# Performance work log

Measured on AMD Instinct MI355X. Metric: run time of the kernel, lower is better.

## Reference

```python
import jax, jax.numpy as jnp
import numpy as np

L, B, T, S, W, H = 4, 2, 2048, 512, 512, 8  # layers, batch, n_ctx, cond units, width, heads
CH = W // H


def _ln(x, g, b):
    m = x.mean(-1, keepdims=True)
    v = ((x - m) ** 2).mean(-1, keepdims=True)
    return (x - m) * jax.lax.rsqrt(v + 1e-5) * g + b


def setup_inputs() -> dict:
    key = jax.random.key(0)
    ks = jax.random.split(key, 16)
    std = 0.25 * np.sqrt(1.0 / W)  # init_scale * sqrt(1/width), as in Transformer.__init__
    f32 = jnp.float32
    d = {
        "x": jax.random.normal(ks[0], (B, T, W), f32),
        "cond_k": jax.random.normal(ks[1], (B, S, W), f32),
        "cond_v": jax.random.normal(ks[2], (B, S, W), f32),
        # stacked per-layer params; weights stored [in, out] (torch Linear transposed)
        "qkv_w": jax.random.normal(ks[3], (L, W, 3 * W), f32) * std,
        "qkv_b": jnp.zeros((L, 3 * W), f32),
        "attn_proj_w": jax.random.normal(ks[4], (L, W, W), f32) * std,
        "attn_proj_b": jnp.zeros((L, W), f32),
        "cross_proj_w": jax.random.normal(ks[5], (L, W, W), f32) * std,
        "cross_proj_b": jnp.zeros((L, W), f32),
        "fc_w": jax.random.normal(ks[6], (L, W, 4 * W), f32) * std,
        "fc_b": jnp.zeros((L, 4 * W), f32),
        "mlp_proj_w": jax.random.normal(ks[7], (L, 4 * W, W), f32) * std,
        "mlp_proj_b": jnp.zeros((L, W), f32),
        "ln1_g": jnp.ones((L, W), f32), "ln1_b": jnp.zeros((L, W), f32),
        "ln3_g": jnp.ones((L, W), f32), "ln3_b": jnp.zeros((L, W), f32),
        "ln4_g": jnp.ones((L, W), f32), "ln4_b": jnp.zeros((L, W), f32),
    }
    return d


def reference(x, cond_k, cond_v, qkv_w, qkv_b, attn_proj_w, attn_proj_b,
              cross_proj_w, cross_proj_b, fc_w, fc_b, mlp_proj_w, mlp_proj_b,
              ln1_g, ln1_b, ln3_g, ln3_b, ln4_g, ln4_b):
    b, t, w = x.shape
    ch = w // H
    scale = 1.0 / np.sqrt(np.sqrt(ch))  # applied to both q and k, as in torch code
    kk = cond_k.reshape(b, -1, H, ch)
    vv = cond_v.reshape(b, -1, H, ch)
    n_layers = qkv_w.shape[0]
    for i in range(n_layers):
        # ---- self-attention ----
        h = _ln(x, ln1_g[i], ln1_b[i])
        qkv = (h @ qkv_w[i] + qkv_b[i]).reshape(b, t, H, 3 * ch)
        q, k, v = qkv[..., :ch], qkv[..., ch:2 * ch], qkv[..., 2 * ch:]
        wts = jnp.einsum('bthc,bshc->bhts', q * scale, k * scale)
        wts = jax.nn.softmax(wts.astype(jnp.float32), axis=-1).astype(wts.dtype)
        a = jnp.einsum('bhts,bshc->bthc', wts, v).reshape(b, t, w)
        x = x + a @ attn_proj_w[i] + attn_proj_b[i]
        # ---- cross-attention (q is ln_3(x) directly, no q projection) ----
        h = _ln(x, ln3_g[i], ln3_b[i])
        q = h.reshape(b, t, H, ch)
        wts = jnp.einsum('bthc,bshc->bhts', q * scale, kk * scale)
        wts = jax.nn.softmax(wts.astype(jnp.float32), axis=-1).astype(wts.dtype)
        a = jnp.einsum('bhts,bshc->bthc', wts, vv).reshape(b, t, w)
        x = x + a @ cross_proj_w[i] + cross_proj_b[i]
        # ---- MLP (exact erf GELU, as torch nn.GELU default) ----
        h = _ln(x, ln4_g[i], ln4_b[i])
        h = jax.nn.gelu(h @ fc_w[i] + fc_b[i], approximate=False)
        x = x + h @ mlp_proj_w[i] + mlp_proj_b[i]
    return x
```

## Files before the change

kernel.cpp:

```cpp
#include <hip/hip_runtime.h>
#include <hip/hip_bf16.h>
#include <cstdint>


typedef __bf16 bf16;
typedef __bf16 bf16x8 __attribute__((ext_vector_type(8)));
typedef float f32x4 __attribute__((ext_vector_type(4)));

#define AS1(p) ((__attribute__((address_space(1))) void*)(uintptr_t)(p))
#define AS3(p) ((__attribute__((address_space(3))) void*)(p))

__device__ __forceinline__ unsigned short bf2us(bf16 v) {
    return __builtin_bit_cast(unsigned short, v);
}

template <int N>
__device__ __forceinline__ void vmbar() {
    if constexpr (N == 0)      asm volatile("s_waitcnt vmcnt(0)\n\ts_barrier" ::: "memory");
    else if constexpr (N == 2) asm volatile("s_waitcnt vmcnt(2)\n\ts_barrier" ::: "memory");
    else if constexpr (N == 5) asm volatile("s_waitcnt vmcnt(5)\n\ts_barrier" ::: "memory");
    else if constexpr (N == 6) asm volatile("s_waitcnt vmcnt(6)\n\ts_barrier" ::: "memory");
    else if constexpr (N == 8) asm volatile("s_waitcnt vmcnt(8)\n\ts_barrier" ::: "memory");
    __builtin_amdgcn_sched_barrier(0);
}
__device__ __forceinline__ void plainbar() {
    asm volatile("s_barrier" ::: "memory");
    __builtin_amdgcn_sched_barrier(0);
}

__global__ __launch_bounds__(256) void ln_kernel(const float* __restrict__ x,
                                                 const float* __restrict__ gam,
                                                 const float* __restrict__ bet,
                                                 bf16* __restrict__ h) {
    int row  = blockIdx.x * 4 + (threadIdx.x >> 6);
    int lane = threadIdx.x & 63;
    const float4* xr = (const float4*)(x + (size_t)row * 512) + lane * 2;
    float4 a = xr[0], b = xr[1];
    float s  = a.x + a.y + a.z + a.w + b.x + b.y + b.z + b.w;
    float ss = a.x * a.x + a.y * a.y + a.z * a.z + a.w * a.w +
               b.x * b.x + b.y * b.y + b.z * b.z + b.w * b.w;
#pragma unroll
    for (int off = 1; off < 64; off <<= 1) {
        s  += __shfl_xor(s, off);
        ss += __shfl_xor(ss, off);
    }
    float mean = s * (1.f / 512.f);
    float var  = ss * (1.f / 512.f) - mean * mean;
    float rstd = rsqrtf(fmaxf(var, 0.f) + 1e-5f);
    const float4* gr = (const float4*)gam + lane * 2;
    const float4* br = (const float4*)bet + lane * 2;
    float4 g0 = gr[0], g1 = gr[1], b0 = br[0], b1 = br[1];
    bf16x8 hv;
    hv[0] = (bf16)((a.x - mean) * rstd * g0.x + b0.x);
    hv[1] = (bf16)((a.y - mean) * rstd * g0.y + b0.y);
    hv[2] = (bf16)((a.z - mean) * rstd * g0.z + b0.z);
    hv[3] = (bf16)((a.w - mean) * rstd * g0.w + b0.w);
    hv[4] = (bf16)((b.x - mean) * rstd * g1.x + b1.x);
    hv[5] = (bf16)((b.y - mean) * rstd * g1.y + b1.y);
    hv[6] = (bf16)((b.z - mean) * rstd * g1.z + b1.z);
    hv[7] = (bf16)((b.w - mean) * rstd * g1.w + b1.w);
    *(bf16x8*)(h + (size_t)row * 512 + lane * 8) = hv;
}

__global__ void wtrans_kernel(const float* __restrict__ in, bf16* __restrict__ out,
                              int K, int N) {
    __shared__ float tile[32][33];
    int n0 = blockIdx.x * 32, k0 = blockIdx.y * 32;
    const float* ip = in + (size_t)blockIdx.z * K * N;
    bf16* op = out + (size_t)blockIdx.z * N * K;
#pragma unroll
    for (int i = threadIdx.y; i < 32; i += 8)
        tile[i][threadIdx.x] = ip[(size_t)(k0 + i) * N + n0 + threadIdx.x];
    __syncthreads();
#pragma unroll
    for (int i = threadIdx.y; i < 32; i += 8)
        op[(size_t)(n0 + i) * K + k0 + threadIdx.x] = (bf16)tile[threadIdx.x][i];
}

__global__ void cvt_kernel(const float* __restrict__ in, bf16* __restrict__ out, int n) {
    int i = (blockIdx.x * 256 + threadIdx.x) * 8;
    if (i + 8 <= n) {
        const float4* p = (const float4*)(in + i);
        float4 a = p[0], b = p[1];
        bf16x8 v;
        v[0] = (bf16)a.x; v[1] = (bf16)a.y; v[2] = (bf16)a.z; v[3] = (bf16)a.w;
        v[4] = (bf16)b.x; v[5] = (bf16)b.y; v[6] = (bf16)b.z; v[7] = (bf16)b.w;
        *(bf16x8*)(out + i) = v;
    }
}

__global__ __launch_bounds__(256) void vtrans_self(const bf16* __restrict__ qkvb,
                                                   bf16* __restrict__ VTs, int T_) {
    __shared__ bf16 tl[64][66];
    int tb = blockIdx.x * 64;
    int bh = blockIdx.y;
    int b = bh >> 3, h = bh & 7;
    int tid = threadIdx.x;
#pragma unroll
    for (int e = 0; e < 2; ++e) {
        int idx = e * 256 + tid;
        int t = idx >> 3, ci = (idx & 7) * 8;
        bf16x8 v = *(const bf16x8*)(qkvb + ((size_t)b * T_ + tb + t) * 1536 +
                                    h * 192 + 128 + ci);
#pragma unroll
        for (int j = 0; j < 8; ++j) tl[ci + j][t] = v[j];
    }
    __syncthreads();
#pragma unroll
    for (int e = 0; e < 2; ++e) {
        int idx = e * 256 + tid;
        int ch = idx >> 3, ti = (idx & 7) * 8;
        bf16x8 v;
#pragma unroll
        for (int j = 0; j < 8; ++j) v[j] = tl[ch][ti + j];
        *(bf16x8*)(VTs + ((size_t)bh * 64 + ch) * T_ + tb + ti) = v;
    }
}

__global__ __launch_bounds__(256) void vtrans_cross(const float* __restrict__ cv,
                                                    bf16* __restrict__ VTc, int S_) {
    __shared__ bf16 tl[64][66];
    int sb = blockIdx.x * 64;
    int bh = blockIdx.y;
    int b = bh >> 3, h = bh & 7;
    int tid = threadIdx.x;
#pragma unroll
    for (int e = 0; e < 4; ++e) {
        int idx = e * 256 + tid;
        int s = idx >> 4, ci = (idx & 15) * 4;
        float4 v = *(const float4*)(cv + ((size_t)b * S_ + sb + s) * 512 + h * 64 + ci);
        tl[ci + 0][s] = (bf16)v.x; tl[ci + 1][s] = (bf16)v.y;
        tl[ci + 2][s] = (bf16)v.z; tl[ci + 3][s] = (bf16)v.w;
    }
    __syncthreads();
#pragma unroll
    for (int e = 0; e < 2; ++e) {
        int idx = e * 256 + tid;
        int ch = idx >> 3, si = (idx & 7) * 8;
        bf16x8 v;
#pragma unroll
        for (int j = 0; j < 8; ++j) v[j] = tl[ch][si + j];
        *(bf16x8*)(VTc + ((size_t)bh * 64 + ch) * S_ + sb + si) = v;
    }
}

template <int EPI, int BM>
__global__ __launch_bounds__(256) void gemm_kernel(const bf16* __restrict__ A,
                                                   const bf16* __restrict__ Bt,
                                                   const float* __restrict__ bias,
                                                   const float* res, void* out,
                                                   int M, int N, int K) {
    constexpr int MI = BM / 32;
    constexpr int LPW = BM / 32 + 4;
    constexpr int ABYTES = BM * 128;
    __shared__ __align__(16) bf16 As[2 * BM * 64];
    __shared__ __align__(16) bf16 Bs[2 * 128 * 64];
    int tiles_n = N >> 7;
    int bid = blockIdx.x;
    int cpx = gridDim.x >> 3;
    bid = (bid & 7) * cpx + (bid >> 3);
    int bm = bid / tiles_n, bn = bid % tiles_n;
    int tid = threadIdx.x, wave = tid >> 6, lane = tid & 63;
    int wm = wave >> 1, wn = wave & 1;
    int g = lane >> 4, cc = lane & 15;
    f32x4 acc[MI][4] = {};
    const bf16* Ag = A + (size_t)(bm * BM) * K;
    const bf16* Bg = Bt + (size_t)(bn << 7) * K;
    int scol = (tid & 7) * 8;

    auto stage = [&](int k0, int buf) {
#pragma unroll
        for (int e = 0; e < BM / 32; ++e) {
            int row = (e * 256 + tid) >> 3;
            __builtin_amdgcn_global_load_lds(AS1(Ag + (size_t)row * K + k0 + scol),
                                             AS3((char*)As + buf * ABYTES + e * 4096 + wave * 1024),
                                             16, 0, 0);
        }
#pragma unroll
        for (int e = 0; e < 4; ++e) {
            int row = (e * 256 + tid) >> 3;
            __builtin_amdgcn_global_load_lds(AS1(Bg + (size_t)row * K + k0 + scol),
                                             AS3((char*)Bs + buf * 16384 + e * 4096 + wave * 1024),
                                             16, 0, 0);
        }
    };

    int nk = K >> 6;
    stage(0, 0);
    stage(64, 1);
    for (int t = 0; t < nk; ++t) {
        if (t + 1 < nk) vmbar<LPW>(); else vmbar<0>();
        const bf16* Ab = As + (t & 1) * (BM * 64);
        const bf16* Bb = Bs + (t & 1) * (128 * 64);
#pragma unroll
        for (int kk = 0; kk < 2; ++kk) {
            bf16x8 af[MI], bfr[4];
#pragma unroll
            for (int mi = 0; mi < MI; ++mi)
                af[mi] = *(const bf16x8*)(Ab + (wm * (BM / 2) + mi * 16 + cc) * 64 + kk * 32 + g * 8);
#pragma unroll
            for (int ni = 0; ni < 4; ++ni)
                bfr[ni] = *(const bf16x8*)(Bb + (wn * 64 + ni * 16 + cc) * 64 + kk * 32 + g * 8);
#pragma unroll
            for (int mi = 0; mi < MI; ++mi)
#pragma unroll
                for (int ni = 0; ni < 4; ++ni)
                    acc[mi][ni] = __builtin_amdgcn_mfma_f32_16x16x32_bf16(
                        af[mi], bfr[ni], acc[mi][ni], 0, 0, 0);
        }
        plainbar();
        if (t + 2 < nk) stage((t + 2) * 64, t & 1);
    }
    int m0 = bm * BM + wm * (BM / 2);
    int n0 = (bn << 7) + wn * 64;
#pragma unroll
    for (int ni = 0; ni < 4; ++ni) {
        int n = n0 + ni * 16 + cc;
        float bv = bias[n];
#pragma unroll
        for (int mi = 0; mi < MI; ++mi) {
#pragma unroll
            for (int r = 0; r < 4; ++r) {
                int m = m0 + mi * 16 + g * 4 + r;
                float v = acc[mi][ni][r] + bv;
                if (EPI == 1) v = 0.5f * v * (1.f + erff(v * 0.70710678118654752f));
                if (EPI == 2)
                    ((float*)out)[(size_t)m * N + n] = res[(size_t)m * N + n] + v;
                else
                    ((bf16*)out)[(size_t)m * N + n] = (bf16)v;
            }
        }
    }
}

__global__ __launch_bounds__(512) void attn_kernel(
    const bf16* __restrict__ Qp, int q_rs, int q_hs,
    const bf16* __restrict__ Kp, int k_rs, int k_hs,
    const bf16* __restrict__ Vt, int vt_s,
    bf16* __restrict__ Op, int T_, int S_) {
    __shared__ __align__(16) char SM[40960];

    int numQ = T_ >> 6;
    int phys = blockIdx.x;
    int cpx = gridDim.x >> 3;
    int bid = (phys & 7) * cpx + (phys >> 3);
    int qb = bid % numQ;
    int bh = bid / numQ;
    int b = bh >> 3, h = bh & 7;
    int tid = threadIdx.x, wave = tid >> 6, lane = tid & 63;
    int wq = wave >> 1, ws = wave & 1;
    int g = lane >> 4, cc = lane & 15;
    int qrow0 = qb * 64;
    int swz = (cc >> 1) & 3;

    const bf16* Qb = Qp + ((size_t)b * T_ + qrow0 + wq * 16) * q_rs + h * q_hs;
    const bf16* Kb = Kp + ((size_t)b * S_) * k_rs + h * k_hs;
    const bf16* Vtb = Vt + (size_t)bh * 64 * vt_s;

    const float QSC = 0.125f * 1.44269504088896f;
    bf16x8 qf[2];
#pragma unroll
    for (int kk = 0; kk < 2; ++kk) {
        bf16x8 raw = *(const bf16x8*)(Qb + (size_t)cc * q_rs + kk * 32 + g * 8);
        bf16x8 sc;
#pragma unroll
        for (int j = 0; j < 8; ++j) sc[j] = (bf16)((float)raw[j] * QSC);
        qf[kk] = sc;
    }

    float l_acc = 0.f;
    f32x4 o_acc[4] = {};
    char* Pw = SM + 32768 + wave * 1024;

    auto stage = [&](int s0, int buf) {
        int row = tid >> 3, cp = tid & 7;
        int col = (cp ^ (row & 7)) * 8;
        __builtin_amdgcn_global_load_lds(AS1(Kb + (size_t)(s0 + row) * k_rs + col),
                                         AS3(SM + buf * 8192 + wave * 1024), 16, 0, 0);
        __builtin_amdgcn_global_load_lds(AS1(Vtb + (size_t)row * vt_s + s0 + col),
                                         AS3(SM + 16384 + buf * 8192 + wave * 1024), 16, 0, 0);
    };

    int nt = S_ >> 6;
    stage(0, 0);
    stage(64, 1);
    for (int t = 0; t < nt; ++t) {
        if (t + 1 < nt) vmbar<2>(); else vmbar<0>();
        char* kbc = SM + (t & 1) * 8192;
        char* vbc = SM + 16384 + (t & 1) * 8192;
        f32x4 sf[2] = {};
        __builtin_amdgcn_s_setprio(1);
#pragma unroll
        for (int kk = 0; kk < 2; ++kk)
#pragma unroll
            for (int sn = 0; sn < 2; ++sn) {
                int row = ws * 32 + sn * 16 + cc;
                bf16x8 kf = *(const bf16x8*)(kbc + row * 128 + (((kk * 4 + g) ^ (cc & 7)) << 4));
                sf[sn] = __builtin_amdgcn_mfma_f32_16x16x32_bf16(kf, qf[kk], sf[sn], 0, 0, 0);
            }
        __builtin_amdgcn_s_setprio(0);
#pragma unroll
        for (int sn = 0; sn < 2; ++sn) {
            float p0 = exp2f(sf[sn][0]), p1 = exp2f(sf[sn][1]);
            float p2 = exp2f(sf[sn][2]), p3 = exp2f(sf[sn][3]);
            l_acc += (p0 + p1) + (p2 + p3);
            uint32_t u01 = (uint32_t)bf2us((bf16)p0) | ((uint32_t)bf2us((bf16)p1) << 16);
            uint32_t u23 = (uint32_t)bf2us((bf16)p2) | ((uint32_t)bf2us((bf16)p3) << 16);
            char* pb = Pw + cc * 64 + (((sn * 2 + (g >> 1)) ^ swz) << 4) + (g & 1) * 8;
            uint2 uu; uu.x = u01; uu.y = u23;
            *(uint2*)pb = uu;
        }
        __builtin_amdgcn_s_setprio(1);
        bf16x8 pa = *(const bf16x8*)(Pw + cc * 64 + ((g ^ swz) << 4));
#pragma unroll
        for (int ni = 0; ni < 4; ++ni) {
            int vrow = ni * 16 + cc;
            bf16x8 vf = *(const bf16x8*)(vbc + vrow * 128 + (((ws * 4 + g) ^ (cc & 7)) << 4));
            o_acc[ni] = __builtin_amdgcn_mfma_f32_16x16x32_bf16(pa, vf, o_acc[ni], 0, 0, 0);
        }
        __builtin_amdgcn_s_setprio(0);
        plainbar();
        if (t + 2 < nt) stage((t + 2) * 64, t & 1);
    }

    l_acc += __shfl_xor(l_acc, 16);
    l_acc += __shfl_xor(l_acc, 32);
    float* sco = (float*)SM;
    float* lf = (float*)(SM + 32768);
    float* scw = sco + wave * 1024;
#pragma unroll
    for (int ni = 0; ni < 4; ++ni)
#pragma unroll
        for (int r = 0; r < 4; ++r)
            scw[(4 * g + r) * 64 + ni * 16 + cc] = o_acc[ni][r];
    if (g == 0) lf[wave * 16 + cc] = l_acc;
    __syncthreads();
    int q = tid >> 3, c0 = (tid & 7) * 8;
    int wqq = q >> 4, qr = q & 15;
    float l = lf[(wqq * 2) * 16 + qr] + lf[(wqq * 2 + 1) * 16 + qr];
    float inv = 1.f / l;
    const float* p0p = sco + (wqq * 2) * 1024 + qr * 64 + c0;
    const float* p1p = sco + (wqq * 2 + 1) * 1024 + qr * 64 + c0;
    bf16x8 o1;
#pragma unroll
    for (int e = 0; e < 2; ++e) {
        float4 v0 = *(const float4*)(p0p + e * 4);
        float4 v1 = *(const float4*)(p1p + e * 4);
        o1[e * 4 + 0] = (bf16)((v0.x + v1.x) * inv);
        o1[e * 4 + 1] = (bf16)((v0.y + v1.y) * inv);
        o1[e * 4 + 2] = (bf16)((v0.z + v1.z) * inv);
        o1[e * 4 + 3] = (bf16)((v0.w + v1.w) * inv);
    }
    *(bf16x8*)(Op + ((size_t)b * T_ + qrow0 + q) * 512 + h * 64 + c0) = o1;
}

extern "C" void kernel_launch(void* const* d_in, const int* in_sizes, int n_in,
                              void* d_out, int out_size, void* d_ws, size_t ws_size,
                              hipStream_t stream) {
    const float* x_in    = (const float*)d_in[0];
    const float* cond_k  = (const float*)d_in[1];
    const float* cond_v  = (const float*)d_in[2];
    const float* qkv_w   = (const float*)d_in[3];
    const float* qkv_b   = (const float*)d_in[4];
    const float* attn_w  = (const float*)d_in[5];
    const float* attn_b  = (const float*)d_in[6];
    const float* cross_w = (const float*)d_in[7];
    const float* cross_b = (const float*)d_in[8];
    const float* fc_w    = (const float*)d_in[9];
    const float* fc_b    = (const float*)d_in[10];
    const float* mlp_w   = (const float*)d_in[11];
    const float* mlp_b   = (const float*)d_in[12];
    const float* ln1_g   = (const float*)d_in[13];
    const float* ln1_b   = (const float*)d_in[14];
    const float* ln3_g   = (const float*)d_in[15];
    const float* ln3_b   = (const float*)d_in[16];
    const float* ln4_g   = (const float*)d_in[17];
    const float* ln4_b   = (const float*)d_in[18];

    const int L = 4, T = 2048, S = 512, W = 512;
    const int M = 2 * T;

    char* ws = (char*)d_ws;
    size_t off = 0;
    auto carve = [&](size_t bytes) -> char* {
        char* p = ws + off;
        off += (bytes + 255) & ~(size_t)255;
        return p;
    };
    bf16* wqkv  = (bf16*)carve((size_t)L * 1536 * 512 * 2);
    bf16* wattn = (bf16*)carve((size_t)L * 512 * 512 * 2);
    bf16* wcrs  = (bf16*)carve((size_t)L * 512 * 512 * 2);
    bf16* wfc   = (bf16*)carve((size_t)L * 2048 * 512 * 2);
    bf16* wmlp  = (bf16*)carve((size_t)L * 512 * 2048 * 2);
    bf16* ckb   = (bf16*)carve((size_t)2 * S * W * 2);
    bf16* VTs   = (bf16*)carve((size_t)16 * 64 * T * 2);
    bf16* VTc   = (bf16*)carve((size_t)16 * 64 * S * 2);
    bf16* hbuf  = (bf16*)carve((size_t)M * 512 * 2);
    bf16* qkvb  = (bf16*)carve((size_t)M * 1536 * 2);
    bf16* abuf  = (bf16*)carve((size_t)M * 512 * 2);
    bf16* fcb   = (bf16*)carve((size_t)M * 2048 * 2);

    dim3 tb(32, 8);
    wtrans_kernel<<<dim3(1536 / 32, 512 / 32, L), tb, 0, stream>>>(qkv_w, wqkv, 512, 1536);
    wtrans_kernel<<<dim3(512 / 32, 512 / 32, L), tb, 0, stream>>>(attn_w, wattn, 512, 512);
    wtrans_kernel<<<dim3(512 / 32, 512 / 32, L), tb, 0, stream>>>(cross_w, wcrs, 512, 512);
    wtrans_kernel<<<dim3(2048 / 32, 512 / 32, L), tb, 0, stream>>>(fc_w, wfc, 512, 2048);
    wtrans_kernel<<<dim3(512 / 32, 2048 / 32, L), tb, 0, stream>>>(mlp_w, wmlp, 2048, 512);
    cvt_kernel<<<(2 * S * W) / 2048, 256, 0, stream>>>(cond_k, ckb, 2 * S * W);
    vtrans_cross<<<dim3(S / 64, 16), 256, 0, stream>>>(cond_v, VTc, S);

    float* x = (float*)d_out;
    hipMemcpyAsync(x, (const void*)x_in, (size_t)M * W * sizeof(float),
                   hipMemcpyDeviceToDevice, stream);

    const int nAttn = 16 * (T / 64);
    for (int i = 0; i < L; ++i) {
        ln_kernel<<<M / 4, 256, 0, stream>>>(x, ln1_g + i * 512, ln1_b + i * 512, hbuf);
        gemm_kernel<0, 64><<<(M / 64) * (1536 / 128), 256, 0, stream>>>(
            hbuf, wqkv + (size_t)i * 1536 * 512, qkv_b + i * 1536, nullptr, qkvb,
            M, 1536, 512);
        vtrans_self<<<dim3(T / 64, 16), 256, 0, stream>>>(qkvb, VTs, T);
        attn_kernel<<<nAttn, 512, 0, stream>>>(
            qkvb, 1536, 192, qkvb + 64, 1536, 192, VTs, T,
            abuf, T, T);
        gemm_kernel<2, 32><<<(M / 32) * (512 / 128), 256, 0, stream>>>(
            abuf, wattn + (size_t)i * 512 * 512, attn_b + i * 512, x, x,
            M, 512, 512);
        ln_kernel<<<M / 4, 256, 0, stream>>>(x, ln3_g + i * 512, ln3_b + i * 512, hbuf);
        attn_kernel<<<nAttn, 512, 0, stream>>>(
            hbuf, 512, 64, ckb, 512, 64, VTc, S,
            abuf, T, S);
        gemm_kernel<2, 32><<<(M / 32) * (512 / 128), 256, 0, stream>>>(
            abuf, wcrs + (size_t)i * 512 * 512, cross_b + i * 512, x, x,
            M, 512, 512);
        ln_kernel<<<M / 4, 256, 0, stream>>>(x, ln4_g + i * 512, ln4_b + i * 512, hbuf);
        gemm_kernel<1, 128><<<(M / 128) * (2048 / 128), 256, 0, stream>>>(
            hbuf, wfc + (size_t)i * 2048 * 512, fc_b + i * 2048, nullptr, fcb,
            M, 2048, 512);
        gemm_kernel<2, 32><<<(M / 32) * (512 / 128), 256, 0, stream>>>(
            fcb, wmlp + (size_t)i * 512 * 2048, mlp_b + i * 512, x, x,
            M, 512, 2048);
    }
}
```

Measured before the change: 639.0 us.

## Restructure cross-attention wave tiling to share K/V fragments across two query tiles

Measured after the change: 645.9 us. About the same (+1.1%).

```diff
diff --git a/kernel.cpp b/kernel.cpp
--- a/kernel.cpp
+++ b/kernel.cpp
@@ -17,7 +17,6 @@
 template <int N>
 __device__ __forceinline__ void vmbar() {
     if constexpr (N == 0)      asm volatile("s_waitcnt vmcnt(0)\n\ts_barrier" ::: "memory");
-    else if constexpr (N == 2) asm volatile("s_waitcnt vmcnt(2)\n\ts_barrier" ::: "memory");
     else if constexpr (N == 5) asm volatile("s_waitcnt vmcnt(5)\n\ts_barrier" ::: "memory");
     else if constexpr (N == 6) asm volatile("s_waitcnt vmcnt(6)\n\ts_barrier" ::: "memory");
     else if constexpr (N == 8) asm volatile("s_waitcnt vmcnt(8)\n\ts_barrier" ::: "memory");
@@ -25,6 +24,10 @@
 }
 __device__ __forceinline__ void plainbar() {
     asm volatile("s_barrier" ::: "memory");
+    __builtin_amdgcn_sched_barrier(0);
+}
+__device__ __forceinline__ void ldsbar() {
+    asm volatile("s_waitcnt lgkmcnt(0)\n\ts_barrier" ::: "memory");
     __builtin_amdgcn_sched_barrier(0);
 }
 
@@ -248,29 +251,31 @@
     int bh = bid / numQ;
     int b = bh >> 3, h = bh & 7;
     int tid = threadIdx.x, wave = tid >> 6, lane = tid & 63;
-    int wq = wave >> 1, ws = wave & 1;
+    int wq = wave >> 2, ws = wave & 3;
+    int sh = ws >> 1, nh = ws & 1;
     int g = lane >> 4, cc = lane & 15;
     int qrow0 = qb * 64;
-    int swz = (cc >> 1) & 3;
-
-    const bf16* Qb = Qp + ((size_t)b * T_ + qrow0 + wq * 16) * q_rs + h * q_hs;
+
+    const bf16* Qb = Qp + ((size_t)b * T_ + qrow0 + wq * 32) * q_rs + h * q_hs;
     const bf16* Kb = Kp + ((size_t)b * S_) * k_rs + h * k_hs;
     const bf16* Vtb = Vt + (size_t)bh * 64 * vt_s;
+    char* PB = SM + 32768;
 
     const float QSC = 0.125f * 1.44269504088896f;
-    bf16x8 qf[2];
-#pragma unroll
-    for (int kk = 0; kk < 2; ++kk) {
-        bf16x8 raw = *(const bf16x8*)(Qb + (size_t)cc * q_rs + kk * 32 + g * 8);
-        bf16x8 sc;
-#pragma unroll
-        for (int j = 0; j < 8; ++j) sc[j] = (bf16)((float)raw[j] * QSC);
-        qf[kk] = sc;
-    }
-
-    float l_acc = 0.f;
-    f32x4 o_acc[4] = {};
-    char* Pw = SM + 32768 + wave * 1024;
+    bf16x8 qf[2][2];
+#pragma unroll
+    for (int qn = 0; qn < 2; ++qn)
+#pragma unroll
+        for (int kk = 0; kk < 2; ++kk) {
+            bf16x8 raw = *(const bf16x8*)(Qb + (size_t)(qn * 16 + cc) * q_rs + kk * 32 + g * 8);
+            bf16x8 sc;
+#pragma unroll
+            for (int j = 0; j < 8; ++j) sc[j] = (bf16)((float)raw[j] * QSC);
+            qf[qn][kk] = sc;
+        }
+
+    float l_acc[2] = {0.f, 0.f};
+    f32x4 o_acc[2][2] = {};
 
     auto stage = [&](int s0, int buf) {
         int row = tid >> 3, cp = tid & 7;
@@ -281,66 +286,89 @@
                                          AS3(SM + 16384 + buf * 8192 + wave * 1024), 16, 0, 0);
     };
 
+    stage(0, 0);
+    __syncthreads();
+
     int nt = S_ >> 6;
-    stage(0, 0);
-    stage(64, 1);
+    int cur = 0;
     for (int t = 0; t < nt; ++t) {
-        if (t + 1 < nt) vmbar<2>(); else vmbar<0>();
-        char* kbc = SM + (t & 1) * 8192;
-        char* vbc = SM + 16384 + (t & 1) * 8192;
+        if (t + 1 < nt) stage((t + 1) * 64, cur ^ 1);
+        char* kbc = SM + cur * 8192;
+        char* vbc = SM + 16384 + cur * 8192;
         f32x4 sf[2] = {};
         __builtin_amdgcn_s_setprio(1);
 #pragma unroll
-        for (int kk = 0; kk < 2; ++kk)
-#pragma unroll
-            for (int sn = 0; sn < 2; ++sn) {
-                int row = ws * 32 + sn * 16 + cc;
-                bf16x8 kf = *(const bf16x8*)(kbc + row * 128 + (((kk * 4 + g) ^ (cc & 7)) << 4));
-                sf[sn] = __builtin_amdgcn_mfma_f32_16x16x32_bf16(kf, qf[kk], sf[sn], 0, 0, 0);
-            }
+        for (int kk = 0; kk < 2; ++kk) {
+            int krow = ws * 16 + cc;
+            bf16x8 kf = *(const bf16x8*)(kbc + krow * 128 + (((kk * 4 + g) ^ (krow & 7)) << 4));
+#pragma unroll
+            for (int qn = 0; qn < 2; ++qn)
+                sf[qn] = __builtin_amdgcn_mfma_f32_16x16x32_bf16(kf, qf[qn][kk], sf[qn], 0, 0, 0);
+        }
         __builtin_amdgcn_s_setprio(0);
 #pragma unroll
-        for (int sn = 0; sn < 2; ++sn) {
-            float p0 = exp2f(sf[sn][0]), p1 = exp2f(sf[sn][1]);
-            float p2 = exp2f(sf[sn][2]), p3 = exp2f(sf[sn][3]);
-            l_acc += (p0 + p1) + (p2 + p3);
+        for (int qn = 0; qn < 2; ++qn) {
+            float p0 = exp2f(sf[qn][0]), p1 = exp2f(sf[qn][1]);
+            float p2 = exp2f(sf[qn][2]), p3 = exp2f(sf[qn][3]);
+            l_acc[qn] += (p0 + p1) + (p2 + p3);
             uint32_t u01 = (uint32_t)bf2us((bf16)p0) | ((uint32_t)bf2us((bf16)p1) << 16);
             uint32_t u23 = (uint32_t)bf2us((bf16)p2) | ((uint32_t)bf2us((bf16)p3) << 16);
-            char* pb = Pw + cc * 64 + (((sn * 2 + (g >> 1)) ^ swz) << 4) + (g & 1) * 8;
+            int prow = wq * 32 + qn * 16 + cc;
+            int chunk = ws * 2 + (g >> 1);
+            char* pb = PB + prow * 128 + ((chunk ^ (prow & 7)) << 4) + (g & 1) * 8;
             uint2 uu; uu.x = u01; uu.y = u23;
             *(uint2*)pb = uu;
         }
+        ldsbar();
         __builtin_amdgcn_s_setprio(1);
-        bf16x8 pa = *(const bf16x8*)(Pw + cc * 64 + ((g ^ swz) << 4));
-#pragma unroll
-        for (int ni = 0; ni < 4; ++ni) {
-            int vrow = ni * 16 + cc;
-            bf16x8 vf = *(const bf16x8*)(vbc + vrow * 128 + (((ws * 4 + g) ^ (cc & 7)) << 4));
-            o_acc[ni] = __builtin_amdgcn_mfma_f32_16x16x32_bf16(pa, vf, o_acc[ni], 0, 0, 0);
-        }
+        bf16x8 pa[2], vf[2];
+#pragma unroll
+        for (int qn = 0; qn < 2; ++qn) {
+            int prow = wq * 32 + qn * 16 + cc;
+            pa[qn] = *(const bf16x8*)(PB + prow * 128 + (((sh * 4 + g) ^ (prow & 7)) << 4));
+        }
+#pragma unroll
+        for (int nj = 0; nj < 2; ++nj) {
+            int vrow = (nh * 2 + nj) * 16 + cc;
+            vf[nj] = *(const bf16x8*)(vbc + vrow * 128 + (((sh * 4 + g) ^ (vrow & 7)) << 4));
+        }
+#pragma unroll
+        for (int qn = 0; qn < 2; ++qn)
+#pragma unroll
+            for (int nj = 0; nj < 2; ++nj)
+                o_acc[qn][nj] = __builtin_amdgcn_mfma_f32_16x16x32_bf16(
+                    pa[qn], vf[nj], o_acc[qn][nj], 0, 0, 0);
         __builtin_amdgcn_s_setprio(0);
-        plainbar();
-        if (t + 2 < nt) stage((t + 2) * 64, t & 1);
-    }
-
-    l_acc += __shfl_xor(l_acc, 16);
-    l_acc += __shfl_xor(l_acc, 32);
+        __syncthreads();
+        cur ^= 1;
+    }
+
+#pragma unroll
+    for (int qn = 0; qn < 2; ++qn) {
+        l_acc[qn] += __shfl_xor(l_acc[qn], 16);
+        l_acc[qn] += __shfl_xor(l_acc[qn], 32);
+    }
     float* sco = (float*)SM;
-    float* lf = (float*)(SM + 32768);
+    float* lf  = (float*)(SM + 32768);
     float* scw = sco + wave * 1024;
 #pragma unroll
-    for (int ni = 0; ni < 4; ++ni)
-#pragma unroll
-        for (int r = 0; r < 4; ++r)
-            scw[(4 * g + r) * 64 + ni * 16 + cc] = o_acc[ni][r];
-    if (g == 0) lf[wave * 16 + cc] = l_acc;
+    for (int qn = 0; qn < 2; ++qn) {
+        if (g == 0) lf[wave * 32 + qn * 16 + cc] = l_acc[qn];
+#pragma unroll
+        for (int nj = 0; nj < 2; ++nj)
+#pragma unroll
+            for (int r = 0; r < 4; ++r)
+                scw[(qn * 16 + 4 * g + r) * 32 + nj * 16 + cc] = o_acc[qn][nj][r];
+    }
     __syncthreads();
     int q = tid >> 3, c0 = (tid & 7) * 8;
-    int wqq = q >> 4, qr = q & 15;
-    float l = lf[(wqq * 2) * 16 + qr] + lf[(wqq * 2 + 1) * 16 + qr];
+    int wqq = q >> 5, qr = q & 31;
+    int nhh = c0 >> 5, chl = c0 & 31;
+    float l = lf[(wqq * 4 + 0) * 32 + qr] + lf[(wqq * 4 + 1) * 32 + qr] +
+              lf[(wqq * 4 + 2) * 32 + qr] + lf[(wqq * 4 + 3) * 32 + qr];
     float inv = 1.f / l;
-    const float* p0p = sco + (wqq * 2) * 1024 + qr * 64 + c0;
-    const float* p1p = sco + (wqq * 2 + 1) * 1024 + qr * 64 + c0;
+    const float* p0p = sco + (wqq * 4 + 0 * 2 + nhh) * 1024 + qr * 32 + chl;
+    const float* p1p = sco + (wqq * 4 + 1 * 2 + nhh) * 1024 + qr * 32 + chl;
     bf16x8 o1;
 #pragma unroll
     for (int e = 0; e < 2; ++e) {
```

## Double KV tile to 128 keys per iteration in attention kernel

Applied to the files above, without the earlier changes.

Measured after the change: 638.5 us. About the same (-0.1%).

```diff
diff --git a/kernel.cpp b/kernel.cpp
--- a/kernel.cpp
+++ b/kernel.cpp
@@ -17,7 +17,6 @@
 template <int N>
 __device__ __forceinline__ void vmbar() {
     if constexpr (N == 0)      asm volatile("s_waitcnt vmcnt(0)\n\ts_barrier" ::: "memory");
-    else if constexpr (N == 2) asm volatile("s_waitcnt vmcnt(2)\n\ts_barrier" ::: "memory");
     else if constexpr (N == 5) asm volatile("s_waitcnt vmcnt(5)\n\ts_barrier" ::: "memory");
     else if constexpr (N == 6) asm volatile("s_waitcnt vmcnt(6)\n\ts_barrier" ::: "memory");
     else if constexpr (N == 8) asm volatile("s_waitcnt vmcnt(8)\n\ts_barrier" ::: "memory");
@@ -238,7 +237,7 @@
     const bf16* __restrict__ Kp, int k_rs, int k_hs,
     const bf16* __restrict__ Vt, int vt_s,
     bf16* __restrict__ Op, int T_, int S_) {
-    __shared__ __align__(16) char SM[40960];
+    __shared__ __align__(16) char SM[81920];
 
     int numQ = T_ >> 6;
     int phys = blockIdx.x;
@@ -251,7 +250,7 @@
     int wq = wave >> 1, ws = wave & 1;
     int g = lane >> 4, cc = lane & 15;
     int qrow0 = qb * 64;
-    int swz = (cc >> 1) & 3;
+    int swz = cc & 7;
 
     const bf16* Qb = Qp + ((size_t)b * T_ + qrow0 + wq * 16) * q_rs + h * q_hs;
     const bf16* Kb = Kp + ((size_t)b * S_) * k_rs + h * k_hs;
@@ -270,63 +269,79 @@
 
     float l_acc = 0.f;
     f32x4 o_acc[4] = {};
-    char* Pw = SM + 32768 + wave * 1024;
+    char* Pw = SM + 65536 + wave * 2048;
 
     auto stage = [&](int s0, int buf) {
-        int row = tid >> 3, cp = tid & 7;
-        int col = (cp ^ (row & 7)) * 8;
-        __builtin_amdgcn_global_load_lds(AS1(Kb + (size_t)(s0 + row) * k_rs + col),
-                                         AS3(SM + buf * 8192 + wave * 1024), 16, 0, 0);
-        __builtin_amdgcn_global_load_lds(AS1(Vtb + (size_t)row * vt_s + s0 + col),
-                                         AS3(SM + 16384 + buf * 8192 + wave * 1024), 16, 0, 0);
+#pragma unroll
+        for (int e = 0; e < 2; ++e) {
+            int L = e * 512 + tid;
+            int row = L >> 3, cp = L & 7;
+            int col = (cp ^ (row & 7)) * 8;
+            __builtin_amdgcn_global_load_lds(AS1(Kb + (size_t)(s0 + row) * k_rs + col),
+                                             AS3(SM + buf * 16384 + e * 8192 + wave * 1024), 16, 0, 0);
+        }
+#pragma unroll
+        for (int e = 0; e < 2; ++e) {
+            int L = e * 512 + tid;
+            int row = L >> 4, cp = L & 15;
+            int scl = (cp ^ (row & 15)) * 8;
+            __builtin_amdgcn_global_load_lds(AS1(Vtb + (size_t)row * vt_s + s0 + scl),
+                                             AS3(SM + 32768 + buf * 16384 + e * 8192 + wave * 1024), 16, 0, 0);
+        }
     };
 
-    int nt = S_ >> 6;
     stage(0, 0);
-    stage(64, 1);
+    __syncthreads();
+
+    int nt = S_ >> 7;
+    int cur = 0;
     for (int t = 0; t < nt; ++t) {
-        if (t + 1 < nt) vmbar<2>(); else vmbar<0>();
-        char* kbc = SM + (t & 1) * 8192;
-        char* vbc = SM + 16384 + (t & 1) * 8192;
-        f32x4 sf[2] = {};
+        if (t + 1 < nt) stage((t + 1) * 128, cur ^ 1);
+        char* kbc = SM + cur * 16384;
+        char* vbc = SM + 32768 + cur * 16384;
+        f32x4 sf[4] = {};
         __builtin_amdgcn_s_setprio(1);
 #pragma unroll
         for (int kk = 0; kk < 2; ++kk)
 #pragma unroll
-            for (int sn = 0; sn < 2; ++sn) {
-                int row = ws * 32 + sn * 16 + cc;
-                bf16x8 kf = *(const bf16x8*)(kbc + row * 128 + (((kk * 4 + g) ^ (cc & 7)) << 4));
+            for (int sn = 0; sn < 4; ++sn) {
+                int row = ws * 64 + sn * 16 + cc;
+                bf16x8 kf = *(const bf16x8*)(kbc + row * 128 + (((kk * 4 + g) ^ (row & 7)) << 4));
                 sf[sn] = __builtin_amdgcn_mfma_f32_16x16x32_bf16(kf, qf[kk], sf[sn], 0, 0, 0);
             }
         __builtin_amdgcn_s_setprio(0);
 #pragma unroll
-        for (int sn = 0; sn < 2; ++sn) {
+        for (int sn = 0; sn < 4; ++sn) {
             float p0 = exp2f(sf[sn][0]), p1 = exp2f(sf[sn][1]);
             float p2 = exp2f(sf[sn][2]), p3 = exp2f(sf[sn][3]);
             l_acc += (p0 + p1) + (p2 + p3);
             uint32_t u01 = (uint32_t)bf2us((bf16)p0) | ((uint32_t)bf2us((bf16)p1) << 16);
             uint32_t u23 = (uint32_t)bf2us((bf16)p2) | ((uint32_t)bf2us((bf16)p3) << 16);
-            char* pb = Pw + cc * 64 + (((sn * 2 + (g >> 1)) ^ swz) << 4) + (g & 1) * 8;
+            char* pb = Pw + cc * 128 + (((sn * 2 + (g >> 1)) ^ swz) << 4) + (g & 1) * 8;
             uint2 uu; uu.x = u01; uu.y = u23;
             *(uint2*)pb = uu;
         }
         __builtin_amdgcn_s_setprio(1);
-        bf16x8 pa = *(const bf16x8*)(Pw + cc * 64 + ((g ^ swz) << 4));
-#pragma unroll
-        for (int ni = 0; ni < 4; ++ni) {
-            int vrow = ni * 16 + cc;
-            bf16x8 vf = *(const bf16x8*)(vbc + vrow * 128 + (((ws * 4 + g) ^ (cc & 7)) << 4));
-            o_acc[ni] = __builtin_amdgcn_mfma_f32_16x16x32_bf16(pa, vf, o_acc[ni], 0, 0, 0);
+#pragma unroll
+        for (int kk = 0; kk < 2; ++kk) {
+            bf16x8 pa = *(const bf16x8*)(Pw + cc * 128 + (((kk * 4 + g) ^ swz) << 4));
+#pragma unroll
+            for (int ni = 0; ni < 4; ++ni) {
+                int vrow = ni * 16 + cc;
+                bf16x8 vf = *(const bf16x8*)(vbc + vrow * 256 +
+                                             (((ws * 8 + kk * 4 + g) ^ (vrow & 15)) << 4));
+                o_acc[ni] = __builtin_amdgcn_mfma_f32_16x16x32_bf16(pa, vf, o_acc[ni], 0, 0, 0);
+            }
         }
         __builtin_amdgcn_s_setprio(0);
-        plainbar();
-        if (t + 2 < nt) stage((t + 2) * 64, t & 1);
+        __syncthreads();
+        cur ^= 1;
     }
 
     l_acc += __shfl_xor(l_acc, 16);
     l_acc += __shfl_xor(l_acc, 32);
     float* sco = (float*)SM;
-    float* lf = (float*)(SM + 32768);
+    float* lf = (float*)(SM + 65536);
     float* scw = sco + wave * 1024;
 #pragma unroll
     for (int ni = 0; ni < 4; ++ni)
```
